# Kernel optimization log

Measured on AMD Instinct MI355X. Metric: run time of the kernel, lower is better.

## Reference

```python
import jax, jax.numpy as jnp
import numpy as np

NUM_HEADS = 8
D_MODEL = 256
DIM = D_MODEL // NUM_HEADS  # 32
EPS = 1e-6


def _proj(x, W, b):
    # Conv1d with kernel_size=1 == channel-mixing matmul over length axis
    return jnp.einsum('oi,bil->bol', W, x) + b[None, :, None]


def _linear_attention(q, k, v):
    # q,k,v: [B, dim, heads, L]
    q = jax.nn.elu(q) + 1.0
    k = jax.nn.elu(k) + 1.0
    L = v.shape[3]
    v = v / L
    # KV: [B, dim_v, dim_k, heads]
    KV = jnp.einsum('bdhm,bqhm->bqdh', k, v)
    # Z: [B, heads, L]
    Z = 1.0 / (jnp.einsum('bdhm,bdh->bhm', q, k.sum(3)) + EPS)
    # out: [B, dim, heads, L]
    return jnp.einsum('bdhm,bqdh,bhm->bqhm', q, KV, Z) * L


def setup_inputs() -> dict:
    key = jax.random.key(0)
    ks = jax.random.split(key, 11)
    B, L = 8, 4096
    s = 0.05
    return {
        'query': jax.random.normal(ks[0], (B, D_MODEL, L), dtype=jnp.float32),
        'key':   jax.random.normal(ks[1], (B, D_MODEL, L), dtype=jnp.float32),
        'value': jax.random.normal(ks[2], (B, D_MODEL, L), dtype=jnp.float32),
        'Wq': jax.random.normal(ks[3], (D_MODEL, D_MODEL), dtype=jnp.float32) * s,
        'bq': jnp.zeros((D_MODEL,), dtype=jnp.float32),
        'Wk': jax.random.normal(ks[4], (D_MODEL, D_MODEL), dtype=jnp.float32) * s,
        'bk': jnp.zeros((D_MODEL,), dtype=jnp.float32),
        'Wv': jax.random.normal(ks[5], (D_MODEL, D_MODEL), dtype=jnp.float32) * s,
        'bv': jnp.zeros((D_MODEL,), dtype=jnp.float32),
        'Wm': jax.random.normal(ks[6], (D_MODEL, D_MODEL), dtype=jnp.float32) * s,
        'bm': jnp.zeros((D_MODEL,), dtype=jnp.float32),
    }


def reference(query, key, value, Wq, bq, Wk, bk, Wv, bv, Wm, bm):
    B = query.shape[0]
    q = _proj(query, Wq, bq).reshape(B, DIM, NUM_HEADS, -1)
    k = _proj(key,   Wk, bk).reshape(B, DIM, NUM_HEADS, -1)
    v = _proj(value, Wv, bv).reshape(B, DIM, NUM_HEADS, -1)
    x = _linear_attention(q, k, v)           # [B, dim, heads, L]
    x = x.reshape(B, D_MODEL, -1)            # merge heads back to channels
    return jnp.einsum('oi,bil->bol', Wm, x) + bm[None, :, None]
```

## Files before the change

kernel.cpp:

```cpp
#include <hip/hip_runtime.h>
#include <math.h>

#define D_MODEL 256
#define NHEADS 8
#define HDIM 32
#define BATCH 8
#define SEQL 4096
#define EPS 1e-6f

typedef _Float16 f16;
typedef _Float16 f16x2 __attribute__((ext_vector_type(2)));
typedef _Float16 f16x4 __attribute__((ext_vector_type(4)));
typedef _Float16 f16x8 __attribute__((ext_vector_type(8)));
typedef float f32x4 __attribute__((ext_vector_type(4)));

__device__ __forceinline__ float elu1(float x) {
    return x > 0.f ? x + 1.f : __expf(x);
}

__global__ void prep_kernel(const float* __restrict__ Wq, const float* __restrict__ Wk,
                            const float* __restrict__ Wv, const float* __restrict__ Wm,
                            const float* __restrict__ bq, const float* __restrict__ bk,
                            const float* __restrict__ bv,
                            f16* __restrict__ w16, float* __restrict__ bperm) {
    const int bid = blockIdx.x;
    if (bid < 1024) {
        int idx = bid * 256 + threadIdx.x;
        int mat = idx >> 16;
        int r = idx & 65535;
        int e = r & 7;
        int lane = (r >> 3) & 63;
        int kstep = (r >> 9) & 7;
        int ostrip = r >> 12;
        int o = ostrip * 16 + (lane & 15);
        int k = kstep * 32 + (lane >> 4) * 8 + e;
        const float* W = (mat == 0) ? Wq : (mat == 1) ? Wk : (mat == 2) ? Wv : Wm;
        float v;
        if (mat < 3) v = W[(size_t)(((o & 31) << 3) + (o >> 5)) * 256 + k];
        else         v = W[(size_t)o * 256 + (((k & 31) << 3) + (k >> 5))];
        w16[idx] = (f16)v;
    } else {
        int t = threadIdx.x;
        bperm[0 * 256 + t] = bq[((t & 31) << 3) + (t >> 5)];
        bperm[1 * 256 + t] = bk[((t & 31) << 3) + (t >> 5)];
        bperm[2 * 256 + t] = bv[((t & 31) << 3) + (t >> 5)];
    }
}

#define XSTR 264
__global__ __launch_bounds__(256, 3) void gemm_stage1(
    const float* __restrict__ Xq, const float* __restrict__ Xk, const float* __restrict__ Xv,
    const f16* __restrict__ w16, const float* __restrict__ bperm,
    f16* __restrict__ yq, f16* __restrict__ yk, f16* __restrict__ yv) {
    __shared__ __align__(16) f16 Xs[64 * XSTR];
    f16* Cb = Xs;

    const int z = blockIdx.z;
    const int which = z >> 3;
    const int b = z & 7;
    const float* X = (which == 0) ? Xq : (which == 1) ? Xk : Xv;
    const f16* W = w16 + which * 65536;
    f16* Y = (which == 0) ? yq : (which == 1) ? yk : yv;
    const float* bp = bperm + which * 256;

    const int l0 = blockIdx.x * 64;
    const int tid = threadIdx.x;
    const int wave = tid >> 6, lane = tid & 63;
    const int ln = lane & 15, quad = lane >> 4;
    const int kq = tid >> 4;
    const int lg = tid & 15;

    const float* Xbase = X + ((size_t)(b * D_MODEL) + 4 * kq) * SEQL + l0 + 4 * lg;

    float4 xa[4], xb[4];

#define LOADX(DST, C) do { \
        const float* xp_ = Xbase + (size_t)(64 * (C)) * SEQL; \
        DST[0] = *(const float4*)(xp_ + 0 * SEQL); \
        DST[1] = *(const float4*)(xp_ + 1 * SEQL); \
        DST[2] = *(const float4*)(xp_ + 2 * SEQL); \
        DST[3] = *(const float4*)(xp_ + 3 * SEQL); \
    } while (0)

#define STOREB(SRC, C) do { \
        f16x4 w_; \
        w_[0] = (f16)SRC[0].x; w_[1] = (f16)SRC[1].x; w_[2] = (f16)SRC[2].x; w_[3] = (f16)SRC[3].x; \
        *(f16x4*)&Xs[(4 * lg + 0) * XSTR + 64 * (C) + 4 * kq] = w_; \
        w_[0] = (f16)SRC[0].y; w_[1] = (f16)SRC[1].y; w_[2] = (f16)SRC[2].y; w_[3] = (f16)SRC[3].y; \
        *(f16x4*)&Xs[(4 * lg + 1) * XSTR + 64 * (C) + 4 * kq] = w_; \
        w_[0] = (f16)SRC[0].z; w_[1] = (f16)SRC[1].z; w_[2] = (f16)SRC[2].z; w_[3] = (f16)SRC[3].z; \
        *(f16x4*)&Xs[(4 * lg + 2) * XSTR + 64 * (C) + 4 * kq] = w_; \
        w_[0] = (f16)SRC[0].w; w_[1] = (f16)SRC[1].w; w_[2] = (f16)SRC[2].w; w_[3] = (f16)SRC[3].w; \
        *(f16x4*)&Xs[(4 * lg + 3) * XSTR + 64 * (C) + 4 * kq] = w_; \
    } while (0)

    f32x4 acc[4][4];
#pragma unroll
    for (int mf = 0; mf < 4; ++mf)
#pragma unroll
        for (int nf = 0; nf < 4; ++nf)
#pragma unroll
            for (int r = 0; r < 4; ++r) acc[mf][nf][r] = 0.f;

    LOADX(xa, 0);
    LOADX(xb, 1);
    STOREB(xa, 0);
    LOADX(xa, 2);
    STOREB(xb, 1);
    LOADX(xb, 3);
    STOREB(xa, 2);
    STOREB(xb, 3);
    __syncthreads();

    const f16* Wl = W + lane * 8;
    f16x8 afc[4], afn[4];
#pragma unroll
    for (int mf = 0; mf < 4; ++mf)
        afc[mf] = *(const f16x8*)(Wl + (wave * 32 + mf * 8 + 0) * 512);
#pragma unroll
    for (int s = 0; s < 8; ++s) {
        const int k0 = s * 32;
        if (s < 7) {
#pragma unroll
            for (int mf = 0; mf < 4; ++mf)
                afn[mf] = *(const f16x8*)(Wl + (wave * 32 + mf * 8 + s + 1) * 512);
        }
        f16x8 bf[4];
#pragma unroll
        for (int nf = 0; nf < 4; ++nf)
            bf[nf] = *(const f16x8*)&Xs[(nf * 16 + ln) * XSTR + k0 + quad * 8];
#pragma unroll
        for (int mf = 0; mf < 4; ++mf)
#pragma unroll
            for (int nf = 0; nf < 4; ++nf)
                acc[mf][nf] = __builtin_amdgcn_mfma_f32_16x16x32_f16(afc[mf], bf[nf], acc[mf][nf], 0, 0, 0);
#pragma unroll
        for (int mf = 0; mf < 4; ++mf) afc[mf] = afn[mf];
    }

    float bv_[4][4];
#pragma unroll
    for (int mf = 0; mf < 4; ++mf)
#pragma unroll
        for (int r = 0; r < 4; ++r)
            bv_[mf][r] = bp[wave * 64 + mf * 16 + quad * 4 + r];
    __syncthreads();
#pragma unroll
    for (int mf = 0; mf < 4; ++mf)
#pragma unroll
        for (int nf = 0; nf < 4; ++nf) {
            f16x4 w;
#pragma unroll
            for (int r = 0; r < 4; ++r) w[r] = (f16)(acc[mf][nf][r] + bv_[mf][r]);
            *(f16x4*)&Cb[(nf * 16 + ln) * XSTR + wave * 64 + mf * 16 + quad * 4] = w;
        }
    __syncthreads();
    {
        const int rw = tid >> 3, sg = tid & 7;
#pragma unroll
        for (int u = 0; u < 8; ++u) {
            const int row = (u & 1) * 32 + rw;
            const int col = (u >> 1) * 64 + sg * 8;
            *(f16x8*)(Y + ((size_t)(b * SEQL + l0 + row)) * 256 + col) =
                *(const f16x8*)&Cb[row * XSTR + col];
        }
    }
#undef LOADX
#undef STOREB
}

#define KVLP 66
#define NSPLIT 16
__global__ __launch_bounds__(256) void kv_mfma(
    const f16* __restrict__ kp, const f16* __restrict__ vp,
    float* __restrict__ KVpart, float* __restrict__ ksum_part) {
    __shared__ __align__(16) f16 kT[32 * KVLP];
    __shared__ __align__(16) f16 vT[48 * KVLP];
    const int ls = blockIdx.x;
    const int bh = blockIdx.y;
    const int b = bh >> 3, h = bh & 7;
    const int t = threadIdx.x;
    const int wave = t >> 6, lane = t & 63;
    const int ln = lane & 15, quad = lane >> 4;
    const int lrow = t >> 2, seg = t & 3;

    {
        const int rr = 32 + (t >> 4), c0 = (t & 15) * 4;
        f16x4 w;
        const f16 one = (f16)1.f, zero = (f16)0.f;
        w[0] = w[1] = w[2] = w[3] = (rr == 32) ? one : zero;
        *(f16x4*)&vT[rr * KVLP + c0] = w;
    }

    const int tiP = wave >> 1, tjP = wave & 1;
    f32x4 accP, accS;
#pragma unroll
    for (int r = 0; r < 4; ++r) { accP[r] = 0.f; accS[r] = 0.f; }

    for (int ch = 0; ch < 4; ++ch) {
        __syncthreads();
        const size_t goff = ((size_t)(b * SEQL + ls * 256 + ch * 64 + lrow)) * 256 + h * 32 + seg * 8;
        f16x8 k8 = *(const f16x8*)(kp + goff);
        f16x8 v8 = *(const f16x8*)(vp + goff);
#pragma unroll
        for (int j = 0; j < 8; ++j) {
            kT[(seg * 8 + j) * KVLP + lrow] = (f16)elu1((float)k8[j]);
            vT[(seg * 8 + j) * KVLP + lrow] = v8[j];
        }
        __syncthreads();
#pragma unroll
        for (int ks = 0; ks < 2; ++ks) {
            const int kc = ks * 32 + quad * 8;
            f16x8 bP = *(const f16x8*)&kT[(tjP * 16 + ln) * KVLP + kc];
            f16x8 aP = *(const f16x8*)&vT[(tiP * 16 + ln) * KVLP + kc];
            accP = __builtin_amdgcn_mfma_f32_16x16x32_f16(aP, bP, accP, 0, 0, 0);
            if (wave < 2) {
                f16x8 aS = *(const f16x8*)&vT[(32 + ln) * KVLP + kc];
                accS = __builtin_amdgcn_mfma_f32_16x16x32_f16(aS, bP, accS, 0, 0, 0);
            }
        }
    }

    float* KVp = KVpart + ((size_t)ls * 64 + bh) * 1024;
#pragma unroll
    for (int r = 0; r < 4; ++r)
        KVp[(tiP * 16 + quad * 4 + r) * 32 + tjP * 16 + ln] = accP[r];
    if (wave < 2 && quad == 0)
        ksum_part[((size_t)ls * 64 + bh) * 32 + tjP * 16 + ln] = accS[0];
}

__global__ __launch_bounds__(256) void kv_reduce(
    const float* __restrict__ KVpart, const float* __restrict__ ksum_part,
    f16* __restrict__ KVaug) {
    const int bh = blockIdx.x;
    const int t = threadIdx.x;
    const float* src = KVpart + (size_t)bh * 1024 + t * 4;
    float ax = 0.f, ay = 0.f, az = 0.f, aw = 0.f;
#pragma unroll
    for (int s = 0; s < NSPLIT; ++s) {
        float4 p = *(const float4*)(src + (size_t)s * 65536);
        ax += p.x; ay += p.y; az += p.z; aw += p.w;
    }
    {
        const int qd = t >> 3, c = t & 7;
        const int nf = qd >> 4, lnq = qd & 15, quad = c >> 1;
        const int lane = quad * 16 + lnq;
        f16x4 w4;
        w4[0] = (f16)ax; w4[1] = (f16)ay; w4[2] = (f16)az; w4[3] = (f16)aw;
        *(f16x4*)&KVaug[((size_t)(bh * 3) + nf) * 512 + lane * 8 + (c & 1) * 4] = w4;
    }
    f16* aug2 = KVaug + ((size_t)(bh * 3) + 2) * 512;
    if (t < 32) {
        float ss = 0.f;
#pragma unroll
        for (int s = 0; s < NSPLIT; ++s)
            ss += ksum_part[((size_t)s * 64 + bh) * 32 + t];
        aug2[(size_t)((t >> 3) * 16) * 8 + (t & 7)] = (f16)ss;
    }
    {
        const int lane2 = t >> 2;
        if ((lane2 & 15) != 0) {
            f16x2 z; z[0] = (f16)0.f; z[1] = (f16)0.f;
            *(f16x2*)&aug2[t * 2] = z;
        }
    }
}

__global__ __launch_bounds__(256) void attn_out_kernel(
    const f16* __restrict__ qp, const f16* __restrict__ KVaug,
    const f16* __restrict__ wm16, const float* __restrict__ bm,
    float* __restrict__ out) {
    __shared__ __align__(16) f16 xs[64 * 264];
    __shared__ float dens[8][64];
    const int b = blockIdx.y;
    const int l0 = blockIdx.x * 64;
    const int t = threadIdx.x;
    const int wave = t >> 6, lane = t & 63;
    const int ln = lane & 15, quad = lane >> 4;

    {
        const int rbase = t >> 5, ch = (t & 31) * 8;
        const f16* qr = qp + ((size_t)(b * SEQL + l0 + rbase)) * 256 + ch;
        f16* dst = &xs[rbase * 264 + ch];
#pragma unroll
        for (int p = 0; p < 8; ++p) {
            f16x8 v = *(const f16x8*)(qr + (size_t)(p * 8) * 256);
            f16x8 w;
#pragma unroll
            for (int j = 0; j < 8; ++j) w[j] = (f16)elu1((float)v[j]);
            *(f16x8*)(dst + p * 8 * 264) = w;
        }
    }
    __syncthreads();
#pragma unroll
    for (int hh = 0; hh < 2; ++hh) {
        const int h = wave * 2 + hh;
        const f16* kvb = KVaug + ((size_t)((b * NHEADS + h) * 3)) * 512 + lane * 8;
        f16x8 a_s[4], b_s[3];
#pragma unroll
        for (int nf = 0; nf < 3; ++nf)
            b_s[nf] = *(const f16x8*)(kvb + nf * 512);
#pragma unroll
        for (int mf = 0; mf < 4; ++mf)
            a_s[mf] = *(const f16x8*)&xs[(mf * 16 + ln) * 264 + h * 32 + quad * 8];
        f32x4 C[4][3];
#pragma unroll
        for (int mf = 0; mf < 4; ++mf)
#pragma unroll
            for (int nf = 0; nf < 3; ++nf) {
#pragma unroll
                for (int r = 0; r < 4; ++r) C[mf][nf][r] = 0.f;
                C[mf][nf] = __builtin_amdgcn_mfma_f32_16x16x32_f16(a_s[mf], b_s[nf], C[mf][nf], 0, 0, 0);
            }
        if (ln == 0) {
#pragma unroll
            for (int mf = 0; mf < 4; ++mf)
#pragma unroll
                for (int r = 0; r < 4; ++r)
                    dens[h][mf * 16 + quad * 4 + r] = C[mf][2][r];
        }
        __syncthreads();
#pragma unroll
        for (int mf = 0; mf < 4; ++mf)
#pragma unroll
            for (int r = 0; r < 4; ++r) {
                const int l = mf * 16 + quad * 4 + r;
                const float rd = __builtin_amdgcn_rcpf(dens[h][l] + EPS);
#pragma unroll
                for (int nf = 0; nf < 2; ++nf)
                    xs[l * 264 + h * 32 + nf * 16 + ln] = (f16)(C[mf][nf][r] * rd);
            }
        __syncthreads();
    }
    f32x4 acc[4][4];
#pragma unroll
    for (int mf = 0; mf < 4; ++mf)
#pragma unroll
        for (int nf = 0; nf < 4; ++nf)
#pragma unroll
            for (int r = 0; r < 4; ++r) acc[mf][nf][r] = 0.f;
    const f16* Wl = wm16 + lane * 8;
    f16x8 afc[4], afn[4];
#pragma unroll
    for (int mf = 0; mf < 4; ++mf)
        afc[mf] = *(const f16x8*)(Wl + (wave * 32 + mf * 8 + 0) * 512);
#pragma unroll
    for (int it = 0; it < 8; ++it) {
        const int k0 = it * 32;
        if (it < 7) {
#pragma unroll
            for (int mf = 0; mf < 4; ++mf)
                afn[mf] = *(const f16x8*)(Wl + (wave * 32 + mf * 8 + it + 1) * 512);
        }
        f16x8 bf[4];
#pragma unroll
        for (int nf = 0; nf < 4; ++nf)
            bf[nf] = *(const f16x8*)&xs[(nf * 16 + ln) * 264 + k0 + quad * 8];
#pragma unroll
        for (int mf = 0; mf < 4; ++mf)
#pragma unroll
            for (int nf = 0; nf < 4; ++nf)
                acc[mf][nf] = __builtin_amdgcn_mfma_f32_16x16x32_f16(afc[mf], bf[nf], acc[mf][nf], 0, 0, 0);
#pragma unroll
        for (int mf = 0; mf < 4; ++mf) afc[mf] = afn[mf];
    }
    float* Of = (float*)xs;
    __syncthreads();
#pragma unroll
    for (int p = 0; p < 2; ++p) {
        if ((wave >> 1) == p) {
            const int rb = (wave & 1) * 64;
#pragma unroll
            for (int mf = 0; mf < 4; ++mf)
#pragma unroll
                for (int r = 0; r < 4; ++r) {
                    const int o = wave * 64 + mf * 16 + quad * 4 + r;
                    const float bb = bm[o];
                    const int row = rb + mf * 16 + quad * 4 + r;
#pragma unroll
                    for (int nf = 0; nf < 4; ++nf)
                        Of[row * 66 + nf * 16 + ln] = acc[mf][nf][r] + bb;
                }
        }
        __syncthreads();
        {
            const int rw = t >> 4, lc = (t & 15) * 4;
#pragma unroll
            for (int rnd = 0; rnd < 8; ++rnd) {
                const int row = rnd * 16 + rw;
                float4 v4 = *(const float4*)&Of[row * 66 + lc];
                *(float4*)(out + ((size_t)(b * D_MODEL + p * 128 + row)) * SEQL + l0 + lc) = v4;
            }
        }
        __syncthreads();
    }
}

extern "C" void kernel_launch(void* const* d_in, const int* in_sizes, int n_in,
                              void* d_out, int out_size, void* d_ws, size_t ws_size,
                              hipStream_t stream) {
    const float* query = (const float*)d_in[0];
    const float* key_  = (const float*)d_in[1];
    const float* value = (const float*)d_in[2];
    const float* Wq = (const float*)d_in[3];
    const float* bq = (const float*)d_in[4];
    const float* Wk = (const float*)d_in[5];
    const float* bk = (const float*)d_in[6];
    const float* Wv = (const float*)d_in[7];
    const float* bv = (const float*)d_in[8];
    const float* Wm = (const float*)d_in[9];
    const float* bm = (const float*)d_in[10];

    char* w = (char*)d_ws;
    f16*   w16    = (f16*)w;
    float* bperm  = (float*)(w + 524288);
    float* KVpart = (float*)(w + 528384);
    float* ksum_p = (float*)(w + 4722688);
    f16*   KVaug  = (f16*)(w + 4853760);
    f16*   qp     = (f16*)(w + 5050368);
    f16*   kp     = qp + (size_t)BATCH * SEQL * 256;
    f16*   vp     = kp + (size_t)BATCH * SEQL * 256;

    prep_kernel<<<1025, 256, 0, stream>>>(Wq, Wk, Wv, Wm, bq, bk, bv, w16, bperm);

    gemm_stage1<<<dim3(SEQL / 64, 1, 24), 256, 0, stream>>>(
        query, key_, value, w16, bperm, qp, kp, vp);

    kv_mfma<<<dim3(NSPLIT, BATCH * NHEADS), 256, 0, stream>>>(kp, vp, KVpart, ksum_p);

    kv_reduce<<<dim3(BATCH * NHEADS), 256, 0, stream>>>(KVpart, ksum_p, KVaug);

    attn_out_kernel<<<dim3(SEQL / 64, BATCH), 256, 0, stream>>>(
        qp, KVaug, w16 + 3 * 65536, bm, (float*)d_out);
}
```

Before: 194.0 us.

## Fuse K/V projections with per-tile KV accumulation into one kernel

Merges the Q/K/V projection GEMM and the KV-product kernel: each block projects K, applies ELU and computes key sums, projects V, then computes per-64-row partial KV matrices from shared memory before projecting Q. This avoids writing and re-reading the fp16 K and V projections through global memory and removes one kernel launch. In exchange the grid shrinks from 24x to 8x along z with serialized work per block and 2 blocks/CU occupancy, and the KV partials grow to 64 splits, which increases the kv_reduce workload.

New measurement: 197.0 us. No clear change (+1.5%).

```diff
diff --git a/kernel.cpp b/kernel.cpp
--- a/kernel.cpp
+++ b/kernel.cpp
@@ -48,185 +48,223 @@
 }
 
 #define XSTR 264
-__global__ __launch_bounds__(256, 3) void gemm_stage1(
+#define KVS 66
+#define NSPLIT 64
+__global__ __launch_bounds__(256, 2) void gemm_fused(
     const float* __restrict__ Xq, const float* __restrict__ Xk, const float* __restrict__ Xv,
     const f16* __restrict__ w16, const float* __restrict__ bperm,
-    f16* __restrict__ yq, f16* __restrict__ yk, f16* __restrict__ yv) {
-    __shared__ __align__(16) f16 Xs[64 * XSTR];
-    f16* Cb = Xs;
-
-    const int z = blockIdx.z;
-    const int which = z >> 3;
-    const int b = z & 7;
-    const float* X = (which == 0) ? Xq : (which == 1) ? Xk : Xv;
-    const f16* W = w16 + which * 65536;
-    f16* Y = (which == 0) ? yq : (which == 1) ? yk : yv;
-    const float* bp = bperm + which * 256;
-
-    const int l0 = blockIdx.x * 64;
+    f16* __restrict__ qp, float* __restrict__ KVpart, float* __restrict__ ksum_part) {
+    __shared__ __align__(16) f16 BufA[64 * XSTR];
+    __shared__ __align__(16) f16 BufB[64 * XSTR];
+
+    const int b = blockIdx.z;
+    const int ls = blockIdx.x;
+    const int l0 = ls * 64;
     const int tid = threadIdx.x;
     const int wave = tid >> 6, lane = tid & 63;
     const int ln = lane & 15, quad = lane >> 4;
     const int kq = tid >> 4;
     const int lg = tid & 15;
 
-    const float* Xbase = X + ((size_t)(b * D_MODEL) + 4 * kq) * SEQL + l0 + 4 * lg;
+    const size_t xoff = ((size_t)(b * D_MODEL) + 4 * kq) * SEQL + l0 + 4 * lg;
 
     float4 xa[4], xb[4];
 
-#define LOADX(DST, C) do { \
-        const float* xp_ = Xbase + (size_t)(64 * (C)) * SEQL; \
+#define LOADX(DST, XP, C) do { \
+        const float* xp_ = (XP) + xoff + (size_t)(64 * (C)) * SEQL; \
         DST[0] = *(const float4*)(xp_ + 0 * SEQL); \
         DST[1] = *(const float4*)(xp_ + 1 * SEQL); \
         DST[2] = *(const float4*)(xp_ + 2 * SEQL); \
         DST[3] = *(const float4*)(xp_ + 3 * SEQL); \
     } while (0)
 
-#define STOREB(SRC, C) do { \
+#define STOREB(SRC, BUF, C) do { \
         f16x4 w_; \
         w_[0] = (f16)SRC[0].x; w_[1] = (f16)SRC[1].x; w_[2] = (f16)SRC[2].x; w_[3] = (f16)SRC[3].x; \
-        *(f16x4*)&Xs[(4 * lg + 0) * XSTR + 64 * (C) + 4 * kq] = w_; \
+        *(f16x4*)&BUF[(4 * lg + 0) * XSTR + 64 * (C) + 4 * kq] = w_; \
         w_[0] = (f16)SRC[0].y; w_[1] = (f16)SRC[1].y; w_[2] = (f16)SRC[2].y; w_[3] = (f16)SRC[3].y; \
-        *(f16x4*)&Xs[(4 * lg + 1) * XSTR + 64 * (C) + 4 * kq] = w_; \
+        *(f16x4*)&BUF[(4 * lg + 1) * XSTR + 64 * (C) + 4 * kq] = w_; \
         w_[0] = (f16)SRC[0].z; w_[1] = (f16)SRC[1].z; w_[2] = (f16)SRC[2].z; w_[3] = (f16)SRC[3].z; \
-        *(f16x4*)&Xs[(4 * lg + 2) * XSTR + 64 * (C) + 4 * kq] = w_; \
+        *(f16x4*)&BUF[(4 * lg + 2) * XSTR + 64 * (C) + 4 * kq] = w_; \
         w_[0] = (f16)SRC[0].w; w_[1] = (f16)SRC[1].w; w_[2] = (f16)SRC[2].w; w_[3] = (f16)SRC[3].w; \
-        *(f16x4*)&Xs[(4 * lg + 3) * XSTR + 64 * (C) + 4 * kq] = w_; \
+        *(f16x4*)&BUF[(4 * lg + 3) * XSTR + 64 * (C) + 4 * kq] = w_; \
     } while (0)
 
+#define STAGE(XP, BUF) do { \
+        LOADX(xa, XP, 0); \
+        LOADX(xb, XP, 1); \
+        STOREB(xa, BUF, 0); \
+        LOADX(xa, XP, 2); \
+        STOREB(xb, BUF, 1); \
+        LOADX(xb, XP, 3); \
+        STOREB(xa, BUF, 2); \
+        STOREB(xb, BUF, 3); \
+    } while (0)
+
     f32x4 acc[4][4];
-#pragma unroll
-    for (int mf = 0; mf < 4; ++mf)
-#pragma unroll
-        for (int nf = 0; nf < 4; ++nf)
-#pragma unroll
-            for (int r = 0; r < 4; ++r) acc[mf][nf][r] = 0.f;
-
-    LOADX(xa, 0);
-    LOADX(xb, 1);
-    STOREB(xa, 0);
-    LOADX(xa, 2);
-    STOREB(xb, 1);
-    LOADX(xb, 3);
-    STOREB(xa, 2);
-    STOREB(xb, 3);
-    __syncthreads();
-
-    const f16* Wl = W + lane * 8;
-    f16x8 afc[4], afn[4];
-#pragma unroll
-    for (int mf = 0; mf < 4; ++mf)
-        afc[mf] = *(const f16x8*)(Wl + (wave * 32 + mf * 8 + 0) * 512);
-#pragma unroll
-    for (int s = 0; s < 8; ++s) {
-        const int k0 = s * 32;
-        if (s < 7) {
+#define ZEROACC() do { \
+        _Pragma("unroll") for (int mf = 0; mf < 4; ++mf) \
+        _Pragma("unroll") for (int nf = 0; nf < 4; ++nf) \
+        _Pragma("unroll") for (int r = 0; r < 4; ++r) acc[mf][nf][r] = 0.f; \
+    } while (0)
+
+#define COMPUTE(BUF, WMAT) do { \
+        const f16* Wl = (WMAT) + lane * 8; \
+        f16x8 afc[4], afn[4]; \
+        _Pragma("unroll") for (int mf = 0; mf < 4; ++mf) \
+            afc[mf] = *(const f16x8*)(Wl + (wave * 32 + mf * 8 + 0) * 512); \
+        _Pragma("unroll") for (int s = 0; s < 8; ++s) { \
+            const int k0 = s * 32; \
+            if (s < 7) { \
+                _Pragma("unroll") for (int mf = 0; mf < 4; ++mf) \
+                    afn[mf] = *(const f16x8*)(Wl + (wave * 32 + mf * 8 + s + 1) * 512); \
+            } \
+            f16x8 bf[4]; \
+            _Pragma("unroll") for (int nf = 0; nf < 4; ++nf) \
+                bf[nf] = *(const f16x8*)&BUF[(nf * 16 + ln) * XSTR + k0 + quad * 8]; \
+            _Pragma("unroll") for (int mf = 0; mf < 4; ++mf) \
+            _Pragma("unroll") for (int nf = 0; nf < 4; ++nf) \
+                acc[mf][nf] = __builtin_amdgcn_mfma_f32_16x16x32_f16(afc[mf], bf[nf], acc[mf][nf], 0, 0, 0); \
+            _Pragma("unroll") for (int mf = 0; mf < 4; ++mf) afc[mf] = afn[mf]; \
+        } \
+    } while (0)
+
+    STAGE(Xk, BufA);
+    __syncthreads();
+    ZEROACC();
+    COMPUTE(BufA, w16 + 65536);
+    {
+        const float* bpk = bperm + 256;
+        float sp[4][4];
+#pragma unroll
+        for (int mf = 0; mf < 4; ++mf)
+#pragma unroll
+            for (int r = 0; r < 4; ++r) {
+                const int o = wave * 64 + mf * 16 + quad * 4 + r;
+                const float bb = bpk[o];
+                float s = 0.f;
+#pragma unroll
+                for (int nf = 0; nf < 4; ++nf) {
+                    const int l = nf * 16 + ln;
+                    const float e = elu1(acc[mf][nf][r] + bb);
+                    s += e;
+                    BufB[o * KVS + l] = (f16)e;
+                }
+                sp[mf][r] = s;
+            }
+#pragma unroll
+        for (int st = 1; st < 16; st <<= 1)
 #pragma unroll
             for (int mf = 0; mf < 4; ++mf)
-                afn[mf] = *(const f16x8*)(Wl + (wave * 32 + mf * 8 + s + 1) * 512);
-        }
-        f16x8 bf[4];
-#pragma unroll
-        for (int nf = 0; nf < 4; ++nf)
-            bf[nf] = *(const f16x8*)&Xs[(nf * 16 + ln) * XSTR + k0 + quad * 8];
-#pragma unroll
-        for (int mf = 0; mf < 4; ++mf)
-#pragma unroll
-            for (int nf = 0; nf < 4; ++nf)
-                acc[mf][nf] = __builtin_amdgcn_mfma_f32_16x16x32_f16(afc[mf], bf[nf], acc[mf][nf], 0, 0, 0);
-#pragma unroll
-        for (int mf = 0; mf < 4; ++mf) afc[mf] = afn[mf];
-    }
-
-    float bv_[4][4];
-#pragma unroll
-    for (int mf = 0; mf < 4; ++mf)
-#pragma unroll
-        for (int r = 0; r < 4; ++r)
-            bv_[mf][r] = bp[wave * 64 + mf * 16 + quad * 4 + r];
-    __syncthreads();
-#pragma unroll
-    for (int mf = 0; mf < 4; ++mf)
-#pragma unroll
-        for (int nf = 0; nf < 4; ++nf) {
-            f16x4 w;
-#pragma unroll
-            for (int r = 0; r < 4; ++r) w[r] = (f16)(acc[mf][nf][r] + bv_[mf][r]);
-            *(f16x4*)&Cb[(nf * 16 + ln) * XSTR + wave * 64 + mf * 16 + quad * 4] = w;
-        }
-    __syncthreads();
-    {
+#pragma unroll
+                for (int r = 0; r < 4; ++r)
+                    sp[mf][r] += __shfl_xor(sp[mf][r], st);
+        if (ln == 0) {
+#pragma unroll
+            for (int mf = 0; mf < 4; ++mf)
+#pragma unroll
+                for (int r = 0; r < 4; ++r) {
+                    const int o = wave * 64 + mf * 16 + quad * 4 + r;
+                    ksum_part[((size_t)ls * 64 + b * NHEADS + (o >> 5)) * 32 + (o & 31)] = sp[mf][r];
+                }
+        }
+    }
+    __syncthreads();
+
+    STAGE(Xv, BufA);
+    __syncthreads();
+    ZEROACC();
+    COMPUTE(BufA, w16 + 131072);
+    __syncthreads();
+    {
+        const float* bpv = bperm + 512;
+#pragma unroll
+        for (int mf = 0; mf < 4; ++mf)
+#pragma unroll
+            for (int r = 0; r < 4; ++r) {
+                const int o = wave * 64 + mf * 16 + quad * 4 + r;
+                const float bb = bpv[o];
+#pragma unroll
+                for (int nf = 0; nf < 4; ++nf)
+                    BufA[o * KVS + nf * 16 + ln] = (f16)(acc[mf][nf][r] + bb);
+            }
+    }
+    __syncthreads();
+    {
+#pragma unroll
+        for (int hh = 0; hh < 2; ++hh) {
+            const int h = wave * 2 + hh;
+            f32x4 kvacc[2][2];
+#pragma unroll
+            for (int ti = 0; ti < 2; ++ti)
+#pragma unroll
+                for (int tj = 0; tj < 2; ++tj)
+#pragma unroll
+                    for (int r = 0; r < 4; ++r) kvacc[ti][tj][r] = 0.f;
+#pragma unroll
+            for (int ks = 0; ks < 2; ++ks) {
+                const int kc = ks * 32 + quad * 8;
+                f16x8 aV[2], bK[2];
+#pragma unroll
+                for (int tt = 0; tt < 2; ++tt) {
+                    aV[tt] = *(const f16x8*)&BufA[(h * 32 + tt * 16 + ln) * KVS + kc];
+                    bK[tt] = *(const f16x8*)&BufB[(h * 32 + tt * 16 + ln) * KVS + kc];
+                }
+#pragma unroll
+                for (int ti = 0; ti < 2; ++ti)
+#pragma unroll
+                    for (int tj = 0; tj < 2; ++tj)
+                        kvacc[ti][tj] = __builtin_amdgcn_mfma_f32_16x16x32_f16(aV[ti], bK[tj], kvacc[ti][tj], 0, 0, 0);
+            }
+            float* KVp = KVpart + ((size_t)ls * 64 + b * NHEADS + h) * 1024;
+#pragma unroll
+            for (int ti = 0; ti < 2; ++ti)
+#pragma unroll
+                for (int tj = 0; tj < 2; ++tj)
+#pragma unroll
+                    for (int r = 0; r < 4; ++r)
+                        KVp[(ti * 16 + quad * 4 + r) * 32 + tj * 16 + ln] = kvacc[ti][tj][r];
+        }
+    }
+    __syncthreads();
+
+    STAGE(Xq, BufB);
+    __syncthreads();
+    ZEROACC();
+    COMPUTE(BufB, w16);
+    __syncthreads();
+    {
+        const float* bpq = bperm;
+        float bv_[4][4];
+#pragma unroll
+        for (int mf = 0; mf < 4; ++mf)
+#pragma unroll
+            for (int r = 0; r < 4; ++r)
+                bv_[mf][r] = bpq[wave * 64 + mf * 16 + quad * 4 + r];
+#pragma unroll
+        for (int mf = 0; mf < 4; ++mf)
+#pragma unroll
+            for (int nf = 0; nf < 4; ++nf) {
+                f16x4 w;
+#pragma unroll
+                for (int r = 0; r < 4; ++r) w[r] = (f16)(acc[mf][nf][r] + bv_[mf][r]);
+                *(f16x4*)&BufB[(nf * 16 + ln) * XSTR + wave * 64 + mf * 16 + quad * 4] = w;
+            }
+        __syncthreads();
         const int rw = tid >> 3, sg = tid & 7;
 #pragma unroll
         for (int u = 0; u < 8; ++u) {
             const int row = (u & 1) * 32 + rw;
             const int col = (u >> 1) * 64 + sg * 8;
-            *(f16x8*)(Y + ((size_t)(b * SEQL + l0 + row)) * 256 + col) =
-                *(const f16x8*)&Cb[row * XSTR + col];
+            *(f16x8*)(qp + ((size_t)(b * SEQL + l0 + row)) * 256 + col) =
+                *(const f16x8*)&BufB[row * XSTR + col];
         }
     }
 #undef LOADX
 #undef STOREB
-}
-
-#define KVLP 66
-#define NSPLIT 16
-__global__ __launch_bounds__(256) void kv_mfma(
-    const f16* __restrict__ kp, const f16* __restrict__ vp,
-    float* __restrict__ KVpart, float* __restrict__ ksum_part) {
-    __shared__ __align__(16) f16 kT[32 * KVLP];
-    __shared__ __align__(16) f16 vT[48 * KVLP];
-    const int ls = blockIdx.x;
-    const int bh = blockIdx.y;
-    const int b = bh >> 3, h = bh & 7;
-    const int t = threadIdx.x;
-    const int wave = t >> 6, lane = t & 63;
-    const int ln = lane & 15, quad = lane >> 4;
-    const int lrow = t >> 2, seg = t & 3;
-
-    {
-        const int rr = 32 + (t >> 4), c0 = (t & 15) * 4;
-        f16x4 w;
-        const f16 one = (f16)1.f, zero = (f16)0.f;
-        w[0] = w[1] = w[2] = w[3] = (rr == 32) ? one : zero;
-        *(f16x4*)&vT[rr * KVLP + c0] = w;
-    }
-
-    const int tiP = wave >> 1, tjP = wave & 1;
-    f32x4 accP, accS;
-#pragma unroll
-    for (int r = 0; r < 4; ++r) { accP[r] = 0.f; accS[r] = 0.f; }
-
-    for (int ch = 0; ch < 4; ++ch) {
-        __syncthreads();
-        const size_t goff = ((size_t)(b * SEQL + ls * 256 + ch * 64 + lrow)) * 256 + h * 32 + seg * 8;
-        f16x8 k8 = *(const f16x8*)(kp + goff);
-        f16x8 v8 = *(const f16x8*)(vp + goff);
-#pragma unroll
-        for (int j = 0; j < 8; ++j) {
-            kT[(seg * 8 + j) * KVLP + lrow] = (f16)elu1((float)k8[j]);
-            vT[(seg * 8 + j) * KVLP + lrow] = v8[j];
-        }
-        __syncthreads();
-#pragma unroll
-        for (int ks = 0; ks < 2; ++ks) {
-            const int kc = ks * 32 + quad * 8;
-            f16x8 bP = *(const f16x8*)&kT[(tjP * 16 + ln) * KVLP + kc];
-            f16x8 aP = *(const f16x8*)&vT[(tiP * 16 + ln) * KVLP + kc];
-            accP = __builtin_amdgcn_mfma_f32_16x16x32_f16(aP, bP, accP, 0, 0, 0);
-            if (wave < 2) {
-                f16x8 aS = *(const f16x8*)&vT[(32 + ln) * KVLP + kc];
-                accS = __builtin_amdgcn_mfma_f32_16x16x32_f16(aS, bP, accS, 0, 0, 0);
-            }
-        }
-    }
-
-    float* KVp = KVpart + ((size_t)ls * 64 + bh) * 1024;
-#pragma unroll
-    for (int r = 0; r < 4; ++r)
-        KVp[(tiP * 16 + quad * 4 + r) * 32 + tjP * 16 + ln] = accP[r];
-    if (wave < 2 && quad == 0)
-        ksum_part[((size_t)ls * 64 + bh) * 32 + tjP * 16 + ln] = accS[0];
+#undef STAGE
+#undef ZEROACC
+#undef COMPUTE
 }
 
 __global__ __launch_bounds__(256) void kv_reduce(
@@ -415,18 +453,14 @@
     f16*   w16    = (f16*)w;
     float* bperm  = (float*)(w + 524288);
     float* KVpart = (float*)(w + 528384);
-    float* ksum_p = (float*)(w + 4722688);
-    f16*   KVaug  = (f16*)(w + 4853760);
-    f16*   qp     = (f16*)(w + 5050368);
-    f16*   kp     = qp + (size_t)BATCH * SEQL * 256;
-    f16*   vp     = kp + (size_t)BATCH * SEQL * 256;
+    float* ksum_p = (float*)(w + 17305600);
+    f16*   KVaug  = (f16*)(w + 17829888);
+    f16*   qp     = (f16*)(w + 18026496);
 
     prep_kernel<<<1025, 256, 0, stream>>>(Wq, Wk, Wv, Wm, bq, bk, bv, w16, bperm);
 
-    gemm_stage1<<<dim3(SEQL / 64, 1, 24), 256, 0, stream>>>(
-        query, key_, value, w16, bperm, qp, kp, vp);
-
-    kv_mfma<<<dim3(NSPLIT, BATCH * NHEADS), 256, 0, stream>>>(kp, vp, KVpart, ksum_p);
+    gemm_fused<<<dim3(SEQL / 64, 1, BATCH), 256, 0, stream>>>(
+        query, key_, value, w16, bperm, qp, KVpart, ksum_p);
 
     kv_reduce<<<dim3(BATCH * NHEADS), 256, 0, stream>>>(KVpart, ksum_p, KVaug);
 
```
